# Kernel tuning notes

Hardware: AMD Instinct MI355X
Metric: run time of the kernel (lower is better)

The kernel has to match this reference:

```python
import jax, jax.numpy as jnp
import numpy as np

N = 50000      # nodes
E = 800000     # edges (avg degree 16)
DIN = 256      # in_dim
EDIM = 16      # raw edge feature dim
H = 2          # heads
C = 64         # out_dim per head
NEG_SLOPE = 0.2


def setup_inputs() -> dict:
    key = jax.random.key(0)
    ks = jax.random.split(key, 10)
    s = 0.05
    return {
        "x": jax.random.normal(ks[0], (N, DIN), jnp.float32),
        "edge_index": jax.random.randint(ks[1], (2, E), 0, N, dtype=jnp.int64),
        "edge_attr": jax.random.normal(ks[2], (E, EDIM), jnp.float32),
        "W_ep": jax.random.normal(ks[3], (EDIM, DIN), jnp.float32) * s,
        "b_ep": jnp.zeros((DIN,), jnp.float32),
        "W_l": jax.random.normal(ks[4], (DIN, H * C), jnp.float32) * s,
        "b_l": jnp.zeros((H * C,), jnp.float32),
        "W_r": jax.random.normal(ks[5], (DIN, H * C), jnp.float32) * s,
        "b_r": jnp.zeros((H * C,), jnp.float32),
        "W_e": jax.random.normal(ks[6], (DIN, H * C), jnp.float32) * s,
        "att": jax.random.normal(ks[7], (H, C), jnp.float32) * s,
        "bias": jnp.zeros((H * C,), jnp.float32),
    }


def reference(x, edge_index, edge_attr, W_ep, b_ep, W_l, b_l, W_r, b_r, W_e, att, bias):
    src, dst = edge_index[0], edge_index[1]
    # edge_proj: Linear(edge_dim, in_dim)
    ea = edge_attr @ W_ep + b_ep                       # [E, DIN]
    # GATv2 node projections (lin_l -> source/message, lin_r -> target)
    xl = (x @ W_l + b_l).reshape(N, H, C)              # [N, H, C]
    xr = (x @ W_r + b_r).reshape(N, H, C)              # [N, H, C]
    ee = (ea @ W_e).reshape(E, H, C)                   # [E, H, C] (lin_edge, no bias)
    # per-edge combined features
    m = xl[src] + xr[dst] + ee                         # [E, H, C]
    # GATv2 attention score: att . LeakyReLU(m)
    s = jnp.einsum("ehc,hc->eh", jax.nn.leaky_relu(m, NEG_SLOPE), att)  # [E, H]
    # segment softmax over incoming edges of each target node
    smax = jax.ops.segment_max(s, dst, num_segments=N)  # [N, H]
    ex = jnp.exp(s - smax[dst])                         # [E, H]
    denom = jax.ops.segment_sum(ex, dst, num_segments=N)
    alpha = ex / denom[dst]                             # [E, H]
    # weighted scatter-add of source messages (xl[src])
    out = jax.ops.segment_sum(alpha[:, :, None] * xl[src], dst, num_segments=N)  # [N, H, C]
    return out.reshape(N, H * C) + bias
```

## Files before the change

### kernel.cpp

```cpp
#include <hip/hip_runtime.h>
#include <hip/hip_bf16.h>
#include <math.h>

#define DIN 256
#define EDIM 16
#define HC 128
#define GBM 128
#define GBN 256
#define GBK 32
#define LDS_STRIDE 40
#define BSTRIDE 64

typedef __attribute__((ext_vector_type(8))) short short8v;
typedef __attribute__((ext_vector_type(4))) float floatx4;
typedef __attribute__((ext_vector_type(2))) float floatx2;
typedef __attribute__((ext_vector_type(4))) unsigned short ushort4v;
typedef __attribute__((ext_vector_type(2))) int intx2;

__device__ inline unsigned short f2bf(float f) {
    union { float f; unsigned u; } v; v.f = f;
    unsigned r = v.u + 0x7FFF + ((v.u >> 16) & 1);
    return (unsigned short)(r >> 16);
}

__global__ void k_prep(const float* __restrict__ W_ep, const float* __restrict__ b_ep,
                       const float* __restrict__ W_e,
                       float* __restrict__ Wc, float* __restrict__ bc) {
    int tid = blockIdx.x * blockDim.x + threadIdx.x;
    if (tid < EDIM * HC) {
        int k = tid >> 7, j = tid & 127;
        float s = 0.f;
        for (int d = 0; d < DIN; ++d) s += W_ep[k * DIN + d] * W_e[d * HC + j];
        Wc[tid] = s;
    } else if (tid < EDIM * HC + HC) {
        int j = tid - EDIM * HC;
        float s = 0.f;
        for (int d = 0; d < DIN; ++d) s += b_ep[d] * W_e[d * HC + j];
        bc[j] = s;
    }
}

__global__ __launch_bounds__(256) void k_convw(const float* __restrict__ Wl,
                                               const float* __restrict__ Wr,
                                               unsigned short* __restrict__ Wb) {
    __shared__ unsigned short tile[32][33];
    int tx = threadIdx.x & 31, ty = threadIdx.x >> 5;
    int c0 = blockIdx.x * 32, k0 = blockIdx.y * 32;
#pragma unroll
    for (int i = 0; i < 4; ++i) {
        int k = k0 + ty + i * 8;
        int col = c0 + tx;
        float v = (col < HC) ? Wl[(size_t)k * HC + col] : Wr[(size_t)k * HC + (col - HC)];
        tile[ty + i * 8][tx] = f2bf(v);
    }
    __syncthreads();
#pragma unroll
    for (int i = 0; i < 4; ++i) {
        int col = c0 + ty + i * 8;
        int k = k0 + tx;
        Wb[(size_t)col * DIN + k] = tile[tx][ty + i * 8];
    }
}

__global__ __launch_bounds__(256) void k_mm(const float* __restrict__ x,
    const unsigned short* __restrict__ Wb,
    const float* __restrict__ bl, const float* __restrict__ br,
    float* __restrict__ xlp, float* __restrict__ xrp, int M) {
    __shared__ unsigned short As[GBM * LDS_STRIDE];
    __shared__ unsigned short Bs[GBN * LDS_STRIDE];

    int t = threadIdx.x;
    int wid = t >> 6, lane = t & 63;
    int wm = wid >> 1, wn = wid & 1;
    int m0 = blockIdx.x * GBM;

    floatx4 acc[4][8];
#pragma unroll
    for (int i = 0; i < 4; ++i)
#pragma unroll
        for (int j = 0; j < 8; ++j) acc[i][j] = (floatx4){0.f, 0.f, 0.f, 0.f};

    int row_l = lane & 15, kg = (lane >> 4) * 8;

    for (int kb = 0; kb < DIN; kb += GBK) {
#pragma unroll
        for (int j = 0; j < 4; ++j) {
            int c = t + 256 * j;
            int r = c >> 3, kk = (c & 7) * 4;
            int gr = m0 + r; if (gr >= M) gr = M - 1;
            floatx4 v = *(const floatx4*)(x + (size_t)gr * DIN + kb + kk);
            ushort4v u;
            u[0] = f2bf(v[0]); u[1] = f2bf(v[1]); u[2] = f2bf(v[2]); u[3] = f2bf(v[3]);
            *(ushort4v*)(&As[r * LDS_STRIDE + kk]) = u;
        }
#pragma unroll
        for (int j = 0; j < 4; ++j) {
            int c = t + 256 * j;
            int col = c >> 2, kk = (c & 3) * 8;
            short8v v = *(const short8v*)(Wb + (size_t)col * DIN + kb + kk);
            *(short8v*)(&Bs[col * LDS_STRIDE + kk]) = v;
        }
        __syncthreads();

        short8v a[4], b[8];
#pragma unroll
        for (int i = 0; i < 4; ++i)
            a[i] = *(short8v*)(&As[(wm * 64 + i * 16 + row_l) * LDS_STRIDE + kg]);
#pragma unroll
        for (int j = 0; j < 8; ++j)
            b[j] = *(short8v*)(&Bs[(wn * 128 + j * 16 + row_l) * LDS_STRIDE + kg]);
#pragma unroll
        for (int i = 0; i < 4; ++i)
#pragma unroll
            for (int j = 0; j < 8; ++j)
                acc[i][j] = __builtin_amdgcn_mfma_f32_16x16x32_bf16(a[i], b[j], acc[i][j], 0, 0, 0);
        __syncthreads();
    }

    int colf = lane & 15, rq = (lane >> 4) * 4;
#pragma unroll
    for (int j = 0; j < 8; ++j) {
        int col = wn * 128 + j * 16 + colf;
        float* base; int pc; float bs;
        if (col < HC) { base = xlp; pc = col; bs = bl[col]; }
        else          { base = xrp; pc = col - HC; bs = br[pc]; }
        int l = (pc >> 6) * 32 + (pc & 31);
        int slot = (pc >> 5) & 1;
#pragma unroll
        for (int i = 0; i < 4; ++i) {
#pragma unroll
            for (int q = 0; q < 4; ++q) {
                int row = m0 + wm * 64 + i * 16 + rq + q;
                if (row < M) base[((size_t)row * 64 + l) * 2 + slot] = acc[i][j][q] + bs;
            }
        }
    }
}

__global__ void k_scatter(const int* __restrict__ ei, int* __restrict__ cnt,
                          intx2* __restrict__ buckets, int E) {
    int e = blockIdx.x * blockDim.x + threadIdx.x;
    if (e < E) {
        int dst = ei[E + e];
        int pos = atomicAdd(&cnt[dst], 1);
        if (pos < BSTRIDE) {
            intx2 se; se.x = ei[e]; se.y = e;
            buckets[(size_t)dst * BSTRIDE + pos] = se;
        }
    }
}

__global__ __launch_bounds__(128, 4) void k_node(const float* __restrict__ xlp,
    const float* __restrict__ xrp, const float* __restrict__ Wc,
    const float* __restrict__ bc, const float* __restrict__ att,
    const float* __restrict__ bias, const int* __restrict__ cnt,
    const intx2* __restrict__ buckets,
    const float* __restrict__ edge_attr, float* __restrict__ out, int n) {
    int wid = __builtin_amdgcn_readfirstlane(threadIdx.x >> 6);
    int lane = threadIdx.x & 63;
    int node = blockIdx.x * 2 + wid;
    if (node >= n) return;
    int g = lane >> 5;
    int ch_a = g * 64 + (lane & 31);
    int ch_b = ch_a + 32;

    floatx2 wc2[EDIM];
#pragma unroll
    for (int k = 0; k < EDIM; ++k) {
        wc2[k].x = Wc[k * HC + ch_a];
        wc2[k].y = Wc[k * HC + ch_b];
    }
    floatx2 bc2; bc2.x = bc[ch_a]; bc2.y = bc[ch_b];
    const float L2E = 1.44269504f;
    floatx2 att2; att2.x = att[ch_a] * L2E; att2.y = att[ch_b] * L2E;
    floatx2 xr2 = *(const floatx2*)(xrp + ((size_t)node * 64 + lane) * 2);

    int deg = cnt[node]; if (deg > BSTRIDE) deg = BSTRIDE;
    const intx2* __restrict__ bk = buckets + (size_t)node * BSTRIDE;

    int bsrc = 0, beid = 0;
    if (lane < deg) {
        intx2 se = bk[lane];
        bsrc = se.x; beid = se.y;
    }

    float D0 = 0.f, D1 = 0.f;
    floatx2 acc0; acc0.x = 0.f; acc0.y = 0.f;
    floatx2 acc1 = acc0;
    int p = 0;
    for (; p + 1 < deg; p += 2) {
        int s0 = __builtin_amdgcn_readlane(bsrc, p);
        int e0 = __builtin_amdgcn_readlane(beid, p);
        int s1 = __builtin_amdgcn_readlane(bsrc, p + 1);
        int e1 = __builtin_amdgcn_readlane(beid, p + 1);
        floatx2 xl0 = *(const floatx2*)(xlp + ((size_t)s0 * 64 + lane) * 2);
        floatx2 xl1 = *(const floatx2*)(xlp + ((size_t)s1 * 64 + lane) * 2);
        const floatx4* __restrict__ ea0 = (const floatx4*)(edge_attr + (size_t)e0 * EDIM);
        const floatx4* __restrict__ ea1 = (const floatx4*)(edge_attr + (size_t)e1 * EDIM);
        floatx2 ee0 = bc2, ee1 = bc2;
#pragma unroll
        for (int q = 0; q < 4; ++q) {
            floatx4 v0 = ea0[q], v1 = ea1[q];
#pragma unroll
            for (int k = 0; k < 4; ++k) {
                ee0 += v0[k] * wc2[q * 4 + k];
                ee1 += v1[k] * wc2[q * 4 + k];
            }
        }
        floatx2 m0 = xl0 + xr2 + ee0;
        floatx2 m1 = xl1 + xr2 + ee1;
        floatx2 l0, l1;
        l0.x = fmaxf(m0.x, 0.f) + 0.2f * fminf(m0.x, 0.f);
        l0.y = fmaxf(m0.y, 0.f) + 0.2f * fminf(m0.y, 0.f);
        l1.x = fmaxf(m1.x, 0.f) + 0.2f * fminf(m1.x, 0.f);
        l1.y = fmaxf(m1.y, 0.f) + 0.2f * fminf(m1.y, 0.f);
        float sc0 = l0.x * att2.x + l0.y * att2.y;
        float sc1 = l1.x * att2.x + l1.y * att2.y;
#pragma unroll
        for (int d = 1; d < 32; d <<= 1) {
            sc0 += __shfl_xor(sc0, d, 64);
            sc1 += __shfl_xor(sc1, d, 64);
        }
        float w0 = exp2f(sc0), w1 = exp2f(sc1);
        D0 += w0; D1 += w1;
        acc0 += w0 * xl0;
        acc1 += w1 * xl1;
    }
    if (p < deg) {
        int s0 = __builtin_amdgcn_readlane(bsrc, p);
        int e0 = __builtin_amdgcn_readlane(beid, p);
        floatx2 xl0 = *(const floatx2*)(xlp + ((size_t)s0 * 64 + lane) * 2);
        const floatx4* __restrict__ ea0 = (const floatx4*)(edge_attr + (size_t)e0 * EDIM);
        floatx2 ee0 = bc2;
#pragma unroll
        for (int q = 0; q < 4; ++q) {
            floatx4 v0 = ea0[q];
#pragma unroll
            for (int k = 0; k < 4; ++k) ee0 += v0[k] * wc2[q * 4 + k];
        }
        floatx2 m0 = xl0 + xr2 + ee0;
        floatx2 l0;
        l0.x = fmaxf(m0.x, 0.f) + 0.2f * fminf(m0.x, 0.f);
        l0.y = fmaxf(m0.y, 0.f) + 0.2f * fminf(m0.y, 0.f);
        float sc0 = l0.x * att2.x + l0.y * att2.y;
#pragma unroll
        for (int d = 1; d < 32; d <<= 1) sc0 += __shfl_xor(sc0, d, 64);
        float w0 = exp2f(sc0);
        D0 += w0;
        acc0 += w0 * xl0;
    }
    float D = D0 + D1;
    floatx2 acc = acc0 + acc1;
    float invD = (D > 0.f) ? 1.f / D : 0.f;
    out[(size_t)node * HC + ch_a] = acc.x * invD + bias[ch_a];
    out[(size_t)node * HC + ch_b] = acc.y * invD + bias[ch_b];
}

extern "C" void kernel_launch(void* const* d_in, const int* in_sizes, int n_in,
                              void* d_out, int out_size, void* d_ws, size_t ws_size,
                              hipStream_t stream) {
    const float* x    = (const float*)d_in[0];
    const int*   ei   = (const int*)d_in[1];
    const float* eatt = (const float*)d_in[2];
    const float* W_ep = (const float*)d_in[3];
    const float* b_ep = (const float*)d_in[4];
    const float* W_l  = (const float*)d_in[5];
    const float* b_l  = (const float*)d_in[6];
    const float* W_r  = (const float*)d_in[7];
    const float* b_r  = (const float*)d_in[8];
    const float* W_e  = (const float*)d_in[9];
    const float* att  = (const float*)d_in[10];
    const float* bias = (const float*)d_in[11];
    float* out = (float*)d_out;

    const int N = in_sizes[0] / DIN;
    const int E = in_sizes[1] / 2;

    char* w = (char*)d_ws;
    size_t o = 0;
    auto alloc = [&](size_t bytes) {
        o = (o + 255) & ~(size_t)255;
        void* p = w + o;
        o += bytes;
        return p;
    };
    float* xlp         = (float*)alloc((size_t)N * HC * sizeof(float));
    float* xrp         = (float*)alloc((size_t)N * HC * sizeof(float));
    intx2* buckets     = (intx2*)alloc((size_t)N * BSTRIDE * sizeof(intx2));
    unsigned short* Wb = (unsigned short*)alloc((size_t)GBN * DIN * sizeof(unsigned short));
    float* Wc          = (float*)alloc(EDIM * HC * sizeof(float));
    float* bc          = (float*)alloc(HC * sizeof(float));
    int*   cnt         = (int*)alloc((size_t)N * sizeof(int));

    hipMemsetAsync(cnt, 0, (size_t)N * sizeof(int), stream);

    k_prep<<<(EDIM * HC + HC + 255) / 256, 256, 0, stream>>>(W_ep, b_ep, W_e, Wc, bc);
    {
        dim3 g(GBN / 32, DIN / 32);
        k_convw<<<g, 256, 0, stream>>>(W_l, W_r, Wb);
    }

    k_mm<<<(N + GBM - 1) / GBM, 256, 0, stream>>>(x, Wb, b_l, b_r, xlp, xrp, N);

    k_scatter<<<(E + 255) / 256, 256, 0, stream>>>(ei, cnt, buckets, E);

    k_node<<<(N + 1) / 2, 128, 0, stream>>>(xlp, xrp, Wc, bc, att, bias, cnt, buckets,
                                            eatt, out, N);
}
```

Before: 206.6 us.

## Halve GEMM M-tile and pin edge-kernel constants in registers

Reduces the node-projection GEMM tile from 128 to 64 rows. Each of the four warps now owns a 64x64 slice of the 256 output columns, with a 4x4 MFMA accumulator instead of 4x8, and the x tile is loaded with two float4 reads per thread. This cuts register pressure and doubles the number of blocks for better occupancy and load balance, at the cost of reloading the B tile for every 64 rows. It also adds empty inline-asm barriers that force the per-lane edge weights and constants in the attention kernel to stay in VGPRs, so the compiler cannot rematerialise or reload them inside the edge loop.

Result: faster. 195.6 us (-5.3%).

```diff
diff --git a/kernel.cpp b/kernel.cpp
--- a/kernel.cpp
+++ b/kernel.cpp
@@ -5,7 +5,7 @@
 #define DIN 256
 #define EDIM 16
 #define HC 128
-#define GBM 128
+#define GBM 64
 #define GBN 256
 #define GBK 32
 #define LDS_STRIDE 40
@@ -21,6 +21,12 @@
     union { float f; unsigned u; } v; v.f = f;
     unsigned r = v.u + 0x7FFF + ((v.u >> 16) & 1);
     return (unsigned short)(r >> 16);
+}
+
+__device__ inline void pin2(floatx2& v) {
+    double t = __builtin_bit_cast(double, v);
+    asm volatile("" : "+v"(t));
+    v = __builtin_bit_cast(floatx2, t);
 }
 
 __global__ void k_prep(const float* __restrict__ W_ep, const float* __restrict__ b_ep,
@@ -71,27 +77,28 @@
 
     int t = threadIdx.x;
     int wid = t >> 6, lane = t & 63;
-    int wm = wid >> 1, wn = wid & 1;
     int m0 = blockIdx.x * GBM;
 
-    floatx4 acc[4][8];
+    floatx4 acc[4][4];
 #pragma unroll
     for (int i = 0; i < 4; ++i)
 #pragma unroll
-        for (int j = 0; j < 8; ++j) acc[i][j] = (floatx4){0.f, 0.f, 0.f, 0.f};
+        for (int j = 0; j < 4; ++j) acc[i][j] = (floatx4){0.f, 0.f, 0.f, 0.f};
 
     int row_l = lane & 15, kg = (lane >> 4) * 8;
 
     for (int kb = 0; kb < DIN; kb += GBK) {
-#pragma unroll
-        for (int j = 0; j < 4; ++j) {
-            int c = t + 256 * j;
-            int r = c >> 3, kk = (c & 7) * 4;
+        {
+            int r = t >> 2, kk = (t & 3) * 8;
             int gr = m0 + r; if (gr >= M) gr = M - 1;
-            floatx4 v = *(const floatx4*)(x + (size_t)gr * DIN + kb + kk);
-            ushort4v u;
-            u[0] = f2bf(v[0]); u[1] = f2bf(v[1]); u[2] = f2bf(v[2]); u[3] = f2bf(v[3]);
-            *(ushort4v*)(&As[r * LDS_STRIDE + kk]) = u;
+            const float* xp = x + (size_t)gr * DIN + kb + kk;
+            floatx4 v0 = *(const floatx4*)xp;
+            floatx4 v1 = *(const floatx4*)(xp + 4);
+            ushort4v u0, u1;
+            u0[0] = f2bf(v0[0]); u0[1] = f2bf(v0[1]); u0[2] = f2bf(v0[2]); u0[3] = f2bf(v0[3]);
+            u1[0] = f2bf(v1[0]); u1[1] = f2bf(v1[1]); u1[2] = f2bf(v1[2]); u1[3] = f2bf(v1[3]);
+            *(ushort4v*)(&As[r * LDS_STRIDE + kk]) = u0;
+            *(ushort4v*)(&As[r * LDS_STRIDE + kk + 4]) = u1;
         }
 #pragma unroll
         for (int j = 0; j < 4; ++j) {
@@ -102,25 +109,25 @@
         }
         __syncthreads();
 
-        short8v a[4], b[8];
+        short8v a[4], b[4];
 #pragma unroll
         for (int i = 0; i < 4; ++i)
-            a[i] = *(short8v*)(&As[(wm * 64 + i * 16 + row_l) * LDS_STRIDE + kg]);
-#pragma unroll
-        for (int j = 0; j < 8; ++j)
-            b[j] = *(short8v*)(&Bs[(wn * 128 + j * 16 + row_l) * LDS_STRIDE + kg]);
+            a[i] = *(short8v*)(&As[(i * 16 + row_l) * LDS_STRIDE + kg]);
+#pragma unroll
+        for (int j = 0; j < 4; ++j)
+            b[j] = *(short8v*)(&Bs[(wid * 64 + j * 16 + row_l) * LDS_STRIDE + kg]);
 #pragma unroll
         for (int i = 0; i < 4; ++i)
 #pragma unroll
-            for (int j = 0; j < 8; ++j)
+            for (int j = 0; j < 4; ++j)
                 acc[i][j] = __builtin_amdgcn_mfma_f32_16x16x32_bf16(a[i], b[j], acc[i][j], 0, 0, 0);
         __syncthreads();
     }
 
     int colf = lane & 15, rq = (lane >> 4) * 4;
 #pragma unroll
-    for (int j = 0; j < 8; ++j) {
-        int col = wn * 128 + j * 16 + colf;
+    for (int j = 0; j < 4; ++j) {
+        int col = wid * 64 + j * 16 + colf;
         float* base; int pc; float bs;
         if (col < HC) { base = xlp; pc = col; bs = bl[col]; }
         else          { base = xrp; pc = col - HC; bs = br[pc]; }
@@ -130,7 +137,7 @@
         for (int i = 0; i < 4; ++i) {
 #pragma unroll
             for (int q = 0; q < 4; ++q) {
-                int row = m0 + wm * 64 + i * 16 + rq + q;
+                int row = m0 + i * 16 + rq + q;
                 if (row < M) base[((size_t)row * 64 + l) * 2 + slot] = acc[i][j][q] + bs;
             }
         }
@@ -174,6 +181,10 @@
     const float L2E = 1.44269504f;
     floatx2 att2; att2.x = att[ch_a] * L2E; att2.y = att[ch_b] * L2E;
     floatx2 xr2 = *(const floatx2*)(xrp + ((size_t)node * 64 + lane) * 2);
+
+#pragma unroll
+    for (int k = 0; k < EDIM; ++k) pin2(wc2[k]);
+    pin2(bc2); pin2(att2); pin2(xr2);
 
     int deg = cnt[node]; if (deg > BSTRIDE) deg = BSTRIDE;
     const intx2* __restrict__ bk = buckets + (size_t)node * BSTRIDE;
```
